# Kernel tuning notes

Hardware: AMD Instinct MI355X
Metric: run time of the kernel (lower is better)

The kernel has to match this reference:

```python
import jax, jax.numpy as jnp
import numpy as np
import math

B, S, D, H = 4, 2048, 1024, 16
DK = D // H

def setup_inputs() -> dict:
    key = jax.random.key(0)
    ks = jax.random.split(key, 8)
    scale = 1.0 / math.sqrt(D)
    q = jax.random.normal(ks[0], (B, S, D), dtype=jnp.float32)
    k = jax.random.normal(ks[1], (B, S, D), dtype=jnp.float32)
    v = jax.random.normal(ks[2], (B, S, D), dtype=jnp.float32)
    Wq = jax.random.normal(ks[3], (D, D), dtype=jnp.float32) * scale
    Wk = jax.random.normal(ks[4], (D, D), dtype=jnp.float32) * scale
    Wv = jax.random.normal(ks[5], (D, D), dtype=jnp.float32) * scale
    Wo = jax.random.normal(ks[6], (D, D), dtype=jnp.float32) * scale
    # causal mask, broadcast over batch and heads (masked_fill where mask == 0)
    mask = jnp.tril(jnp.ones((S, S), dtype=jnp.int32))[None, None, :, :]
    return {"q": q, "k": k, "v": v, "Wq": Wq, "Wk": Wk, "Wv": Wv, "Wo": Wo, "mask": mask}

def reference(q, k, v, Wq, Wk, Wv, Wo, mask):
    # Linear projections (nn.Linear: x @ W^T), split heads -> [B, H, S, DK]
    def split_heads(x, W):
        y = jnp.einsum('bsd,ed->bse', x, W)
        return y.reshape(x.shape[0], x.shape[1], H, DK).transpose(0, 2, 1, 3)
    qh = split_heads(q, Wq)
    kh = split_heads(k, Wk)
    vh = split_heads(v, Wv)
    scores = jnp.einsum('bhqd,bhkd->bhqk', qh, kh) / math.sqrt(DK)  # [B,H,S,S]
    scores = jnp.where(mask == 0, -jnp.inf, scores)
    p = jax.nn.softmax(scores, axis=-1)
    ctx = jnp.einsum('bhqk,bhkd->bhqd', p, vh)
    ctx = ctx.transpose(0, 2, 1, 3).reshape(q.shape[0], q.shape[1], H * DK)
    return jnp.einsum('bsd,ed->bse', ctx, Wo)
```

## Files before the change

### kernel.cpp

```cpp
#include <hip/hip_runtime.h>

#define BB 4
#define SS 2048
#define DD 1024
#define HH 16
#define DKK 64
#define MTOT (BB * SS)
#define QKV_N (MTOT * DD)
#define W_N (DD * DD)

typedef __attribute__((ext_vector_type(8))) short short8;
typedef __attribute__((ext_vector_type(4))) float f32x4;
typedef __attribute__((ext_vector_type(4))) unsigned short u16x4;
typedef unsigned short ushort_t;

#define GP(p) ((__attribute__((address_space(1))) void*)(p))
#define LP(p) ((__attribute__((address_space(3))) void*)(p))

#if __has_builtin(__builtin_amdgcn_exp2f)
#define EXP2(x) __builtin_amdgcn_exp2f(x)
#else
#define EXP2(x) __expf((x) * 0.6931471805599453f)
#endif
#define QSCALE 0.1803368801111204f

__device__ __forceinline__ ushort_t f2bf(float f) {
    union { float f; unsigned u; } c; c.f = f;
    unsigned r = c.u + 0x7fffu + ((c.u >> 16) & 1u);
    return (ushort_t)(r >> 16);
}

__global__ __launch_bounds__(256)
void cvt2(const float* __restrict__ s0, ushort_t* __restrict__ d0, int n0,
          const float* __restrict__ s1, ushort_t* __restrict__ d1, int n1)
{
    int i = (blockIdx.x * 256 + threadIdx.x) * 4;
    const float* s; ushort_t* d; int off;
    if (i < n0) { s = s0; d = d0; off = i; }
    else        { s = s1; d = d1; off = i - n0; if (off >= n1) return; }
    f32x4 x = *(const f32x4*)(s + off);
    u16x4 h;
    h[0] = f2bf(x[0]); h[1] = f2bf(x[1]); h[2] = f2bf(x[2]); h[3] = f2bf(x[3]);
    *(u16x4*)(d + off) = h;
}

template<int MODE>
__global__ __launch_bounds__(256, 3)
void gemm_db(const ushort_t* __restrict__ A, const ushort_t* __restrict__ W,
             void* __restrict__ out, float scale)
{
    __shared__ ushort_t As[2][128 * 32];
    __shared__ ushort_t Bs[2][128 * 32];

    const int tid  = threadIdx.x;
    const int lane = tid & 63;
    const int w    = tid >> 6;
    const int wm   = w >> 1, wn = w & 1;
    const int l15  = lane & 15, l4 = lane >> 4;
    const int m0   = blockIdx.x * 128;
    const int n0   = blockIdx.y * 128;

    f32x4 acc[4][4] = {};

    auto stage = [&](int kk, int buf) {
        #pragma unroll
        for (int i = 0; i < 2; ++i) {
            int c  = i * 256 + tid;
            int r  = c >> 2;
            int cb = (c & 3) ^ (r & 3);
            __builtin_amdgcn_global_load_lds(
                GP(A + (size_t)(m0 + r) * 1024 + kk + cb * 8), LP(&As[buf][c * 8]), 16, 0, 0);
            __builtin_amdgcn_global_load_lds(
                GP(W + (size_t)(n0 + r) * 1024 + kk + cb * 8), LP(&Bs[buf][c * 8]), 16, 0, 0);
        }
    };

    stage(0, 0);

    for (int it = 0; it < 32; ++it) {
        __syncthreads();
        const ushort_t* Ac = As[it & 1];
        const ushort_t* Bc = Bs[it & 1];
        if (it + 1 < 32) stage((it + 1) * 32, (it + 1) & 1);

        short8 bfr[4];
        #pragma unroll
        for (int ni = 0; ni < 4; ++ni) {
            int row = wn * 64 + ni * 16 + l15;
            bfr[ni] = *(const short8*)(Bc + (row * 4 + (l4 ^ (row & 3))) * 8);
        }
        #pragma unroll
        for (int mi = 0; mi < 4; ++mi) {
            int row = wm * 64 + mi * 16 + l15;
            short8 af = *(const short8*)(Ac + (row * 4 + (l4 ^ (row & 3))) * 8);
            #pragma unroll
            for (int ni = 0; ni < 4; ++ni)
                acc[mi][ni] = __builtin_amdgcn_mfma_f32_16x16x32_bf16(
                    af, bfr[ni], acc[mi][ni], 0, 0, 0);
        }
    }

    #pragma unroll
    for (int mi = 0; mi < 4; ++mi) {
        int rowb = m0 + wm * 64 + mi * 16 + l4 * 4;
        #pragma unroll
        for (int ni = 0; ni < 4; ++ni) {
            int n = n0 + wn * 64 + ni * 16 + l15;
            if constexpr (MODE == 0) {
                int h = n >> 6, dk = n & 63;
                #pragma unroll
                for (int r = 0; r < 4; ++r) {
                    int m = rowb + r, b = m >> 11, s = m & 2047;
                    ((ushort_t*)out)[(((size_t)(b * 16 + h) * 2048 + s) << 6) + dk] =
                        f2bf(acc[mi][ni][r] * scale);
                }
            } else if constexpr (MODE == 1) {
                int h = n >> 6, dk = n & 63;
                int b = rowb >> 11, s0v = rowb & 2047;
                u16x4 hh;
                #pragma unroll
                for (int r = 0; r < 4; ++r) hh[r] = f2bf(acc[mi][ni][r]);
                *(u16x4*)((ushort_t*)out + (((size_t)(b * 16 + h) << 6) + dk) * 2048 + s0v) = hh;
            } else {
                #pragma unroll
                for (int r = 0; r < 4; ++r)
                    ((float*)out)[(size_t)(rowb + r) * 1024 + n] = acc[mi][ni][r];
            }
        }
    }
}

__global__ __launch_bounds__(256, 2)
void attn_fwd5(const ushort_t* __restrict__ Qh, const ushort_t* __restrict__ Kh,
               const ushort_t* __restrict__ Vt, ushort_t* __restrict__ Ctx)
{
    __shared__ ushort_t Kl[2][64 * 64];
    __shared__ ushort_t Vl[2][64 * 64];
    __shared__ ushort_t Pl[4][32][72];

    const int tid  = threadIdx.x;
    const int lane = tid & 63;
    const int w    = tid >> 6;
    const int l15  = lane & 15, l4 = lane >> 4;
    const int idx  = blockIdx.x;
    const int qt   = 15 - (idx >> 6);
    const int bh   = idx & 63;
    const int b    = bh >> 4, h = bh & 15;
    const int q0   = qt * 128;
    const ushort_t* Qb = Qh + (size_t)bh * SS * DKK;
    const ushort_t* Kb = Kh + (size_t)bh * SS * DKK;
    const ushort_t* Vb = Vt + (size_t)bh * DKK * SS;

    short8 qf[2][2];
    #pragma unroll
    for (int qg = 0; qg < 2; ++qg)
        #pragma unroll
        for (int ks = 0; ks < 2; ++ks) {
            int row = q0 + w * 32 + qg * 16 + l15;
            qf[qg][ks] = *(const short8*)(Qb + (size_t)row * 64 + ks * 32 + l4 * 8);
        }

    f32x4 Ot[2][4] = {};
    float m_i[2], l_i[2];
    m_i[0] = m_i[1] = -__builtin_inff();
    l_i[0] = l_i[1] = 0.f;

    auto stage = [&](int k0, ushort_t* Kd, ushort_t* Vd) {
        #pragma unroll
        for (int i = 0; i < 2; ++i) {
            int c  = i * 256 + tid;
            int r  = c >> 3;
            int cb = (c & 7) ^ (r & 7);
            __builtin_amdgcn_global_load_lds(
                GP(Kb + (size_t)(k0 + r) * 64 + cb * 8), LP(Kd + c * 8), 16, 0, 0);
            __builtin_amdgcn_global_load_lds(
                GP(Vb + (size_t)r * 2048 + k0 + cb * 8), LP(Vd + c * 8), 16, 0, 0);
        }
    };

    const int nkt = 2 * qt + 2;
    const int wrow0 = q0 + w * 32;
    stage(0, Kl[0], Vl[0]);

    for (int kt = 0; kt < nkt; ++kt) {
        const int k0 = kt * 64;
        __syncthreads();
        const ushort_t* Kc = Kl[kt & 1];
        const ushort_t* Vc = Vl[kt & 1];
        if (kt + 1 < nkt)
            stage(k0 + 64, Kl[(kt + 1) & 1], Vl[(kt + 1) & 1]);

        f32x4 sc[2][4] = {};
        #pragma unroll
        for (int ni = 0; ni < 4; ++ni) {
            short8 kf0, kf1;
            {
                int r = ni * 16 + l15;
                kf0 = *(const short8*)(Kc + (r * 8 + ((0 + l4) ^ (r & 7))) * 8);
                kf1 = *(const short8*)(Kc + (r * 8 + ((4 + l4) ^ (r & 7))) * 8);
            }
            #pragma unroll
            for (int qg = 0; qg < 2; ++qg) {
                sc[qg][ni] = __builtin_amdgcn_mfma_f32_16x16x32_bf16(
                    kf0, qf[qg][0], sc[qg][ni], 0, 0, 0);
                sc[qg][ni] = __builtin_amdgcn_mfma_f32_16x16x32_bf16(
                    kf1, qf[qg][1], sc[qg][ni], 0, 0, 0);
            }
        }

        if (k0 + 63 > wrow0) {
            #pragma unroll
            for (int qg = 0; qg < 2; ++qg) {
                int qrow = wrow0 + qg * 16 + l15;
                #pragma unroll
                for (int ni = 0; ni < 4; ++ni)
                    #pragma unroll
                    for (int r = 0; r < 4; ++r) {
                        int kcol = k0 + ni * 16 + l4 * 4 + r;
                        if (kcol > qrow) sc[qg][ni][r] = -1.0e30f;
                    }
            }
        }

        #pragma unroll
        for (int qg = 0; qg < 2; ++qg) {
            float mx = sc[qg][0][0];
            #pragma unroll
            for (int ni = 0; ni < 4; ++ni)
                #pragma unroll
                for (int r = 0; r < 4; ++r) mx = fmaxf(mx, sc[qg][ni][r]);
            mx = fmaxf(mx, __shfl_xor(mx, 16, 64));
            mx = fmaxf(mx, __shfl_xor(mx, 32, 64));
            float mnew  = fmaxf(m_i[qg], mx);
            float alpha = EXP2(m_i[qg] - mnew);
            float rs = 0.f;
            #pragma unroll
            for (int ni = 0; ni < 4; ++ni)
                #pragma unroll
                for (int r = 0; r < 4; ++r) {
                    float p = EXP2(sc[qg][ni][r] - mnew);
                    sc[qg][ni][r] = p;
                    rs += p;
                }
            rs += __shfl_xor(rs, 16, 64);
            rs += __shfl_xor(rs, 32, 64);
            l_i[qg] = l_i[qg] * alpha + rs;
            m_i[qg] = mnew;
            #pragma unroll
            for (int nd = 0; nd < 4; ++nd)
                #pragma unroll
                for (int r = 0; r < 4; ++r) Ot[qg][nd][r] *= alpha;
        }

        #pragma unroll
        for (int qg = 0; qg < 2; ++qg) {
            int qr = qg * 16 + l15;
            #pragma unroll
            for (int ni = 0; ni < 4; ++ni) {
                u16x4 hh;
                #pragma unroll
                for (int r = 0; r < 4; ++r) hh[r] = f2bf(sc[qg][ni][r]);
                *(u16x4*)(&Pl[w][qr][ni * 16 + l4 * 4]) = hh;
            }
        }

        short8 pT[2][2];
        #pragma unroll
        for (int qg = 0; qg < 2; ++qg)
            #pragma unroll
            for (int ks = 0; ks < 2; ++ks)
                pT[qg][ks] = *(const short8*)(&Pl[w][qg * 16 + l15][ks * 32 + l4 * 8]);

        #pragma unroll
        for (int nd = 0; nd < 4; ++nd) {
            short8 vf0, vf1;
            {
                int r = nd * 16 + l15;
                vf0 = *(const short8*)(Vc + (r * 8 + ((0 + l4) ^ (r & 7))) * 8);
                vf1 = *(const short8*)(Vc + (r * 8 + ((4 + l4) ^ (r & 7))) * 8);
            }
            #pragma unroll
            for (int qg = 0; qg < 2; ++qg) {
                Ot[qg][nd] = __builtin_amdgcn_mfma_f32_16x16x32_bf16(
                    vf0, pT[qg][0], Ot[qg][nd], 0, 0, 0);
                Ot[qg][nd] = __builtin_amdgcn_mfma_f32_16x16x32_bf16(
                    vf1, pT[qg][1], Ot[qg][nd], 0, 0, 0);
            }
        }
    }

    #pragma unroll
    for (int qg = 0; qg < 2; ++qg) {
        float inv = 1.0f / l_i[qg];
        int qrow = q0 + w * 32 + qg * 16 + l15;
        ushort_t* dst = Ctx + ((size_t)b * 2048 + qrow) * 1024 + h * 64;
        #pragma unroll
        for (int nd = 0; nd < 4; ++nd) {
            u16x4 hh;
            #pragma unroll
            for (int r = 0; r < 4; ++r) hh[r] = f2bf(Ot[qg][nd][r] * inv);
            *(u16x4*)(dst + nd * 16 + l4 * 4) = hh;
        }
    }
}

extern "C" void kernel_launch(void* const* d_in, const int* in_sizes, int n_in,
                              void* d_out, int out_size, void* d_ws, size_t ws_size,
                              hipStream_t stream)
{
    const float* q  = (const float*)d_in[0];
    const float* k  = (const float*)d_in[1];
    const float* v  = (const float*)d_in[2];
    const float* Wq = (const float*)d_in[3];
    const float* Wk = (const float*)d_in[4];
    const float* Wv = (const float*)d_in[5];
    const float* Wo = (const float*)d_in[6];
    float* out = (float*)d_out;

    ushort_t* B0 = (ushort_t*)d_ws;
    ushort_t* B1 = B0 + (size_t)QKV_N;
    ushort_t* B2 = B1 + (size_t)QKV_N;
    ushort_t* B3 = B2 + (size_t)QKV_N;
    ushort_t* wbE = (ushort_t*)d_out;
    dim3 gg(MTOT / 128, DD / 128);
    const int cvtg = (QKV_N + W_N) / 1024;

    cvt2<<<cvtg, 256, 0, stream>>>(q, B0, QKV_N, Wq, wbE, W_N);
    gemm_db<0><<<gg, 256, 0, stream>>>(B0, wbE, B1, QSCALE);

    cvt2<<<cvtg, 256, 0, stream>>>(k, B0, QKV_N, Wk, wbE, W_N);
    gemm_db<0><<<gg, 256, 0, stream>>>(B0, wbE, B2, 1.0f);

    cvt2<<<cvtg, 256, 0, stream>>>(v, B0, QKV_N, Wv, wbE, W_N);
    gemm_db<1><<<gg, 256, 0, stream>>>(B0, wbE, B3, 1.0f);

    attn_fwd5<<<1024, 256, 0, stream>>>(B1, B2, B3, B0);

    cvt2<<<W_N / 1024, 256, 0, stream>>>(Wo, B1, W_N, Wo, B1, 0);
    gemm_db<2><<<gg, 256, 0, stream>>>(B0, B1, out, 1.0f);
}
```

Measured before the change: 340.4 us.

## Batch QKV projections into one GEMM launch and convert fp32 weights inside the GEMM

The three activation fp32->bf16 conversions are merged into one kernel, and the Q/K/V projections into one GEMM launch over a 192x8 grid that picks its input, weight and output layout per segment. The separate weight-conversion kernels are removed: each GEMM now stages fp32 weight tiles into LDS with a new swizzle and packs them to bf16 in registers before the MFMA. This cuts kernel launches and the serial cvt/GEMM dependencies, and gives the projection GEMM a larger grid. In exchange the B-side tile doubles its LDS footprint and global traffic, and every block repeats the weight conversion. Q and K now live in the output buffer as scratch space until the final GEMM overwrites it.

```diff
diff --git a/kernel.cpp b/kernel.cpp
--- a/kernel.cpp
+++ b/kernel.cpp
@@ -30,102 +30,176 @@
     return (ushort_t)(r >> 16);
 }
 
+__device__ __forceinline__ short8 pack8(f32x4 lo, f32x4 hi) {
+    short8 r;
+    r[0] = (short)f2bf(lo[0]); r[1] = (short)f2bf(lo[1]);
+    r[2] = (short)f2bf(lo[2]); r[3] = (short)f2bf(lo[3]);
+    r[4] = (short)f2bf(hi[0]); r[5] = (short)f2bf(hi[1]);
+    r[6] = (short)f2bf(hi[2]); r[7] = (short)f2bf(hi[3]);
+    return r;
+}
+
 __global__ __launch_bounds__(256)
-void cvt2(const float* __restrict__ s0, ushort_t* __restrict__ d0, int n0,
-          const float* __restrict__ s1, ushort_t* __restrict__ d1, int n1)
+void cvt3(const float* __restrict__ q, const float* __restrict__ k,
+          const float* __restrict__ v, ushort_t* __restrict__ qb,
+          ushort_t* __restrict__ kb, ushort_t* __restrict__ vb)
 {
-    int i = (blockIdx.x * 256 + threadIdx.x) * 4;
-    const float* s; ushort_t* d; int off;
-    if (i < n0) { s = s0; d = d0; off = i; }
-    else        { s = s1; d = d1; off = i - n0; if (off >= n1) return; }
+    size_t i = ((size_t)blockIdx.x * 256 + threadIdx.x) * 4;
+    int seg = (int)(i >> 23);
+    size_t off = i & (size_t)(QKV_N - 1);
+    const float* s = (seg == 0) ? q : (seg == 1) ? k : v;
+    ushort_t*    d = (seg == 0) ? qb : (seg == 1) ? kb : vb;
     f32x4 x = *(const f32x4*)(s + off);
     u16x4 h;
     h[0] = f2bf(x[0]); h[1] = f2bf(x[1]); h[2] = f2bf(x[2]); h[3] = f2bf(x[3]);
     *(u16x4*)(d + off) = h;
 }
 
-template<int MODE>
-__global__ __launch_bounds__(256, 3)
-void gemm_db(const ushort_t* __restrict__ A, const ushort_t* __restrict__ W,
-             void* __restrict__ out, float scale)
-{
-    __shared__ ushort_t As[2][128 * 32];
-    __shared__ ushort_t Bs[2][128 * 32];
-
-    const int tid  = threadIdx.x;
-    const int lane = tid & 63;
-    const int w    = tid >> 6;
-    const int wm   = w >> 1, wn = w & 1;
-    const int l15  = lane & 15, l4 = lane >> 4;
-    const int m0   = blockIdx.x * 128;
-    const int n0   = blockIdx.y * 128;
-
-    f32x4 acc[4][4] = {};
-
-    auto stage = [&](int kk, int buf) {
+struct GemmCore {
+    const ushort_t* A; const float* W;
+    int m0, n0, tid, lane, w, wm, wn, l15, l4;
+    ushort_t (*As)[128 * 32];
+    float    (*Bsf)[128 * 32];
+
+    __device__ __forceinline__ void stage(int kk, int buf) {
         #pragma unroll
         for (int i = 0; i < 2; ++i) {
             int c  = i * 256 + tid;
             int r  = c >> 2;
             int cb = (c & 3) ^ (r & 3);
             __builtin_amdgcn_global_load_lds(
-                GP(A + (size_t)(m0 + r) * 1024 + kk + cb * 8), LP(&As[buf][c * 8]), 16, 0, 0);
+                GP(A + (size_t)(m0 + r) * 1024 + kk + cb * 8),
+                LP(&As[buf][c * 8]), 16, 0, 0);
+        }
+        #pragma unroll
+        for (int i = 0; i < 4; ++i) {
+            int c  = i * 256 + tid;
+            int r  = c >> 3;
+            int cb = (c & 7) ^ (r & 7);
             __builtin_amdgcn_global_load_lds(
-                GP(W + (size_t)(n0 + r) * 1024 + kk + cb * 8), LP(&Bs[buf][c * 8]), 16, 0, 0);
-        }
-    };
-
-    stage(0, 0);
-
-    for (int it = 0; it < 32; ++it) {
-        __syncthreads();
-        const ushort_t* Ac = As[it & 1];
-        const ushort_t* Bc = Bs[it & 1];
-        if (it + 1 < 32) stage((it + 1) * 32, (it + 1) & 1);
-
-        short8 bfr[4];
-        #pragma unroll
-        for (int ni = 0; ni < 4; ++ni) {
-            int row = wn * 64 + ni * 16 + l15;
-            bfr[ni] = *(const short8*)(Bc + (row * 4 + (l4 ^ (row & 3))) * 8);
-        }
-        #pragma unroll
-        for (int mi = 0; mi < 4; ++mi) {
-            int row = wm * 64 + mi * 16 + l15;
-            short8 af = *(const short8*)(Ac + (row * 4 + (l4 ^ (row & 3))) * 8);
-            #pragma unroll
-            for (int ni = 0; ni < 4; ++ni)
-                acc[mi][ni] = __builtin_amdgcn_mfma_f32_16x16x32_bf16(
-                    af, bfr[ni], acc[mi][ni], 0, 0, 0);
-        }
-    }
+                GP(W + (size_t)(n0 + r) * 1024 + kk + cb * 4),
+                LP(&Bsf[buf][c * 4]), 16, 0, 0);
+        }
+    }
+
+    __device__ __forceinline__ void run(f32x4 (&acc)[4][4]) {
+        stage(0, 0);
+        for (int it = 0; it < 32; ++it) {
+            __syncthreads();
+            const ushort_t* Ac = As[it & 1];
+            const float*    Bc = Bsf[it & 1];
+            if (it + 1 < 32) stage((it + 1) * 32, (it + 1) & 1);
+
+            short8 bfr[4];
+            #pragma unroll
+            for (int ni = 0; ni < 4; ++ni) {
+                int row = wn * 64 + ni * 16 + l15;
+                f32x4 lo = *(const f32x4*)(&Bc[(row * 8 + ((l4 * 2)     ^ (row & 7))) * 4]);
+                f32x4 hi = *(const f32x4*)(&Bc[(row * 8 + ((l4 * 2 + 1) ^ (row & 7))) * 4]);
+                bfr[ni] = pack8(lo, hi);
+            }
+            #pragma unroll
+            for (int mi = 0; mi < 4; ++mi) {
+                int row = wm * 64 + mi * 16 + l15;
+                short8 af = *(const short8*)(Ac + (row * 4 + (l4 ^ (row & 3))) * 8);
+                #pragma unroll
+                for (int ni = 0; ni < 4; ++ni)
+                    acc[mi][ni] = __builtin_amdgcn_mfma_f32_16x16x32_bf16(
+                        af, bfr[ni], acc[mi][ni], 0, 0, 0);
+            }
+        }
+    }
+};
+
+__global__ __launch_bounds__(256, 3)
+void gemm_qkv(const ushort_t* __restrict__ qb, const ushort_t* __restrict__ kb,
+              const ushort_t* __restrict__ vb, const float* __restrict__ Wq,
+              const float* __restrict__ Wk, const float* __restrict__ Wv,
+              ushort_t* __restrict__ Qh, ushort_t* __restrict__ Kh,
+              ushort_t* __restrict__ Vt)
+{
+    __shared__ ushort_t As[2][128 * 32];
+    __shared__ float    Bsf[2][128 * 32];
+
+    const int tid  = threadIdx.x;
+    const int lane = tid & 63;
+    const int w    = tid >> 6;
+    const int seg  = blockIdx.x >> 6;
+    const int mb   = blockIdx.x & 63;
+
+    GemmCore core;
+    core.A   = (seg == 0) ? qb : (seg == 1) ? kb : vb;
+    core.W   = (seg == 0) ? Wq : (seg == 1) ? Wk : Wv;
+    core.m0  = mb * 128;
+    core.n0  = blockIdx.y * 128;
+    core.tid = tid; core.lane = lane; core.w = w;
+    core.wm  = w >> 1; core.wn = w & 1;
+    core.l15 = lane & 15; core.l4 = lane >> 4;
+    core.As  = As; core.Bsf = Bsf;
+
+    f32x4 acc[4][4] = {};
+    core.run(acc);
+
+    const float scale = (seg == 0) ? QSCALE : 1.0f;
+    ushort_t* outHM = (seg == 0) ? Qh : Kh;
 
     #pragma unroll
     for (int mi = 0; mi < 4; ++mi) {
-        int rowb = m0 + wm * 64 + mi * 16 + l4 * 4;
+        int rowb = core.m0 + core.wm * 64 + mi * 16 + core.l4 * 4;
         #pragma unroll
         for (int ni = 0; ni < 4; ++ni) {
-            int n = n0 + wn * 64 + ni * 16 + l15;
-            if constexpr (MODE == 0) {
-                int h = n >> 6, dk = n & 63;
+            int n = core.n0 + core.wn * 64 + ni * 16 + core.l15;
+            int h = n >> 6, dk = n & 63;
+            if (seg < 2) {
                 #pragma unroll
                 for (int r = 0; r < 4; ++r) {
                     int m = rowb + r, b = m >> 11, s = m & 2047;
-                    ((ushort_t*)out)[(((size_t)(b * 16 + h) * 2048 + s) << 6) + dk] =
+                    outHM[(((size_t)(b * 16 + h) * 2048 + s) << 6) + dk] =
                         f2bf(acc[mi][ni][r] * scale);
                 }
-            } else if constexpr (MODE == 1) {
-                int h = n >> 6, dk = n & 63;
+            } else {
                 int b = rowb >> 11, s0v = rowb & 2047;
                 u16x4 hh;
                 #pragma unroll
                 for (int r = 0; r < 4; ++r) hh[r] = f2bf(acc[mi][ni][r]);
-                *(u16x4*)((ushort_t*)out + (((size_t)(b * 16 + h) << 6) + dk) * 2048 + s0v) = hh;
-            } else {
-                #pragma unroll
-                for (int r = 0; r < 4; ++r)
-                    ((float*)out)[(size_t)(rowb + r) * 1024 + n] = acc[mi][ni][r];
-            }
+                *(u16x4*)(Vt + (((size_t)(b * 16 + h) << 6) + dk) * 2048 + s0v) = hh;
+            }
+        }
+    }
+}
+
+__global__ __launch_bounds__(256, 3)
+void gemm_out(const ushort_t* __restrict__ Ctx, const float* __restrict__ Wo,
+              float* __restrict__ out)
+{
+    __shared__ ushort_t As[2][128 * 32];
+    __shared__ float    Bsf[2][128 * 32];
+
+    const int tid  = threadIdx.x;
+    const int lane = tid & 63;
+    const int w    = tid >> 6;
+
+    GemmCore core;
+    core.A   = Ctx;  core.W = Wo;
+    core.m0  = blockIdx.x * 128;
+    core.n0  = blockIdx.y * 128;
+    core.tid = tid; core.lane = lane; core.w = w;
+    core.wm  = w >> 1; core.wn = w & 1;
+    core.l15 = lane & 15; core.l4 = lane >> 4;
+    core.As  = As; core.Bsf = Bsf;
+
+    f32x4 acc[4][4] = {};
+    core.run(acc);
+
+    #pragma unroll
+    for (int mi = 0; mi < 4; ++mi) {
+        int rowb = core.m0 + core.wm * 64 + mi * 16 + core.l4 * 4;
+        #pragma unroll
+        for (int ni = 0; ni < 4; ++ni) {
+            int n = core.n0 + core.wn * 64 + ni * 16 + core.l15;
+            #pragma unroll
+            for (int r = 0; r < 4; ++r)
+                out[(size_t)(rowb + r) * 1024 + n] = acc[mi][ni][r];
         }
     }
 }
@@ -317,25 +391,16 @@
     const float* Wo = (const float*)d_in[6];
     float* out = (float*)d_out;
 
-    ushort_t* B0 = (ushort_t*)d_ws;
-    ushort_t* B1 = B0 + (size_t)QKV_N;
-    ushort_t* B2 = B1 + (size_t)QKV_N;
-    ushort_t* B3 = B2 + (size_t)QKV_N;
-    ushort_t* wbE = (ushort_t*)d_out;
-    dim3 gg(MTOT / 128, DD / 128);
-    const int cvtg = (QKV_N + W_N) / 1024;
-
-    cvt2<<<cvtg, 256, 0, stream>>>(q, B0, QKV_N, Wq, wbE, W_N);
-    gemm_db<0><<<gg, 256, 0, stream>>>(B0, wbE, B1, QSCALE);
-
-    cvt2<<<cvtg, 256, 0, stream>>>(k, B0, QKV_N, Wk, wbE, W_N);
-    gemm_db<0><<<gg, 256, 0, stream>>>(B0, wbE, B2, 1.0f);
-
-    cvt2<<<cvtg, 256, 0, stream>>>(v, B0, QKV_N, Wv, wbE, W_N);
-    gemm_db<1><<<gg, 256, 0, stream>>>(B0, wbE, B3, 1.0f);
-
-    attn_fwd5<<<1024, 256, 0, stream>>>(B1, B2, B3, B0);
-
-    cvt2<<<W_N / 1024, 256, 0, stream>>>(Wo, B1, W_N, Wo, B1, 0);
-    gemm_db<2><<<gg, 256, 0, stream>>>(B0, B1, out, 1.0f);
-}
+    ushort_t* qb  = (ushort_t*)d_ws;
+    ushort_t* kb  = qb + (size_t)QKV_N;
+    ushort_t* vb  = kb + (size_t)QKV_N;
+    ushort_t* Vt  = vb + (size_t)QKV_N;
+    ushort_t* Ctx = qb;
+    ushort_t* Qh  = (ushort_t*)d_out;
+    ushort_t* Kh  = Qh + (size_t)QKV_N;
+
+    cvt3<<<3 * QKV_N / 1024, 256, 0, stream>>>(q, k, v, qb, kb, vb);
+    gemm_qkv<<<dim3(192, 8), 256, 0, stream>>>(qb, kb, vb, Wq, Wk, Wv, Qh, Kh, Vt);
+    attn_fwd5<<<1024, 256, 0, stream>>>(Qh, Kh, Vt, Ctx);
+    gemm_out<<<dim3(64, 8), 256, 0, stream>>>(Ctx, Wo, out);
+}
```

New measurement: 373.1 us. 1.1x slower.

## Fuse activation bf16 conversion into a single batched QKV GEMM launch

Applied to the files above, without the earlier changes.

Removes the three separate fp32->bf16 conversion passes over q/k/v. The new QKV GEMM loads fp32 activations straight into LDS and packs them to bf16 in registers. The three projections now run as one launch with a 192x8 grid, and all four weight conversions happen in one kernel. The output projection uses 128x64 tiles at higher occupancy, and the attention launch bounds go up to 3 blocks per SM. This saves a lot of global traffic and launch overhead, at the cost of twice the LDS for the A tile and extra conversion ALU work in the GEMM inner loop. Q and K scratch buffers now live in the output buffer.

```diff
diff --git a/kernel.cpp b/kernel.cpp
--- a/kernel.cpp
+++ b/kernel.cpp
@@ -30,27 +30,129 @@
     return (ushort_t)(r >> 16);
 }
 
+__device__ __forceinline__ short8 pack8(f32x4 lo, f32x4 hi) {
+    short8 r;
+    r[0] = (short)f2bf(lo[0]); r[1] = (short)f2bf(lo[1]);
+    r[2] = (short)f2bf(lo[2]); r[3] = (short)f2bf(lo[3]);
+    r[4] = (short)f2bf(hi[0]); r[5] = (short)f2bf(hi[1]);
+    r[6] = (short)f2bf(hi[2]); r[7] = (short)f2bf(hi[3]);
+    return r;
+}
+
 __global__ __launch_bounds__(256)
-void cvt2(const float* __restrict__ s0, ushort_t* __restrict__ d0, int n0,
-          const float* __restrict__ s1, ushort_t* __restrict__ d1, int n1)
+void cvtW(const float* __restrict__ Wq, const float* __restrict__ Wk,
+          const float* __restrict__ Wv, const float* __restrict__ Wo,
+          ushort_t* __restrict__ dst)
 {
     int i = (blockIdx.x * 256 + threadIdx.x) * 4;
-    const float* s; ushort_t* d; int off;
-    if (i < n0) { s = s0; d = d0; off = i; }
-    else        { s = s1; d = d1; off = i - n0; if (off >= n1) return; }
+    int seg = i >> 20;
+    int off = i & (W_N - 1);
+    const float* s = (seg == 0) ? Wq : (seg == 1) ? Wk : (seg == 2) ? Wv : Wo;
     f32x4 x = *(const f32x4*)(s + off);
     u16x4 h;
     h[0] = f2bf(x[0]); h[1] = f2bf(x[1]); h[2] = f2bf(x[2]); h[3] = f2bf(x[3]);
-    *(u16x4*)(d + off) = h;
-}
-
-template<int MODE>
+    *(u16x4*)(dst + i) = h;
+}
+
 __global__ __launch_bounds__(256, 3)
-void gemm_db(const ushort_t* __restrict__ A, const ushort_t* __restrict__ W,
-             void* __restrict__ out, float scale)
+void gemm_qkv(const float* __restrict__ q, const float* __restrict__ k,
+              const float* __restrict__ v, const ushort_t* __restrict__ wb,
+              ushort_t* __restrict__ Qh, ushort_t* __restrict__ Kh,
+              ushort_t* __restrict__ Vt)
+{
+    __shared__ float    Asf[2][128 * 32];
+    __shared__ ushort_t Bs [2][128 * 32];
+
+    const int tid  = threadIdx.x;
+    const int lane = tid & 63;
+    const int w    = tid >> 6;
+    const int wm   = w >> 1, wn = w & 1;
+    const int l15  = lane & 15, l4 = lane >> 4;
+    const int seg  = blockIdx.x >> 6;
+    const int m0   = (blockIdx.x & 63) * 128;
+    const int n0   = blockIdx.y * 128;
+    const float* A = (seg == 0) ? q : (seg == 1) ? k : v;
+    const ushort_t* W = wb + (size_t)seg * W_N;
+
+    auto stage = [&](int kk, int buf) {
+        #pragma unroll
+        for (int i = 0; i < 4; ++i) {
+            int c = i * 256 + tid, r = c >> 3, cb = (c & 7) ^ (r & 7);
+            __builtin_amdgcn_global_load_lds(
+                GP(A + (size_t)(m0 + r) * 1024 + kk + cb * 4),
+                LP(&Asf[buf][c * 4]), 16, 0, 0);
+        }
+        #pragma unroll
+        for (int i = 0; i < 2; ++i) {
+            int c = i * 256 + tid, r = c >> 2, cb = (c & 3) ^ ((r >> 1) & 3);
+            __builtin_amdgcn_global_load_lds(
+                GP(W + (size_t)(n0 + r) * 1024 + kk + cb * 8),
+                LP(&Bs[buf][c * 8]), 16, 0, 0);
+        }
+    };
+
+    f32x4 acc[4][4] = {};
+    stage(0, 0);
+
+    for (int it = 0; it < 32; ++it) {
+        __syncthreads();
+        const float*    Ac = Asf[it & 1];
+        const ushort_t* Bc = Bs[it & 1];
+        if (it + 1 < 32) stage((it + 1) * 32, (it + 1) & 1);
+
+        short8 bfr[4];
+        #pragma unroll
+        for (int ni = 0; ni < 4; ++ni) {
+            int row = wn * 64 + ni * 16 + l15;
+            bfr[ni] = *(const short8*)(Bc + (row * 4 + (l4 ^ ((row >> 1) & 3))) * 8);
+        }
+        #pragma unroll
+        for (int mi = 0; mi < 4; ++mi) {
+            int row = wm * 64 + mi * 16 + l15;
+            f32x4 lo = *(const f32x4*)(&Ac[(row * 8 + ((l4 * 2)     ^ (row & 7))) * 4]);
+            f32x4 hi = *(const f32x4*)(&Ac[(row * 8 + ((l4 * 2 + 1) ^ (row & 7))) * 4]);
+            short8 af = pack8(lo, hi);
+            #pragma unroll
+            for (int ni = 0; ni < 4; ++ni)
+                acc[mi][ni] = __builtin_amdgcn_mfma_f32_16x16x32_bf16(
+                    af, bfr[ni], acc[mi][ni], 0, 0, 0);
+        }
+    }
+
+    const float scale = (seg == 0) ? QSCALE : 1.0f;
+    ushort_t* outHM = (seg == 0) ? Qh : Kh;
+
+    #pragma unroll
+    for (int mi = 0; mi < 4; ++mi) {
+        int rowb = m0 + wm * 64 + mi * 16 + l4 * 4;
+        #pragma unroll
+        for (int ni = 0; ni < 4; ++ni) {
+            int n = n0 + wn * 64 + ni * 16 + l15;
+            int h = n >> 6, dk = n & 63;
+            if (seg < 2) {
+                #pragma unroll
+                for (int r = 0; r < 4; ++r) {
+                    int m = rowb + r, b = m >> 11, s = m & 2047;
+                    outHM[(((size_t)(b * 16 + h) * 2048 + s) << 6) + dk] =
+                        f2bf(acc[mi][ni][r] * scale);
+                }
+            } else {
+                int b = rowb >> 11, s0v = rowb & 2047;
+                u16x4 hh;
+                #pragma unroll
+                for (int r = 0; r < 4; ++r) hh[r] = f2bf(acc[mi][ni][r]);
+                *(u16x4*)(Vt + (((size_t)(b * 16 + h) << 6) + dk) * 2048 + s0v) = hh;
+            }
+        }
+    }
+}
+
+__global__ __launch_bounds__(256, 4)
+void gemm_out(const ushort_t* __restrict__ Ctx, const ushort_t* __restrict__ wo,
+              float* __restrict__ out)
 {
     __shared__ ushort_t As[2][128 * 32];
-    __shared__ ushort_t Bs[2][128 * 32];
+    __shared__ ushort_t Bs[2][64 * 32];
 
     const int tid  = threadIdx.x;
     const int lane = tid & 63;
@@ -58,23 +160,25 @@
     const int wm   = w >> 1, wn = w & 1;
     const int l15  = lane & 15, l4 = lane >> 4;
     const int m0   = blockIdx.x * 128;
-    const int n0   = blockIdx.y * 128;
-
-    f32x4 acc[4][4] = {};
+    const int n0   = blockIdx.y * 64;
 
     auto stage = [&](int kk, int buf) {
         #pragma unroll
         for (int i = 0; i < 2; ++i) {
-            int c  = i * 256 + tid;
-            int r  = c >> 2;
-            int cb = (c & 3) ^ (r & 3);
-            __builtin_amdgcn_global_load_lds(
-                GP(A + (size_t)(m0 + r) * 1024 + kk + cb * 8), LP(&As[buf][c * 8]), 16, 0, 0);
-            __builtin_amdgcn_global_load_lds(
-                GP(W + (size_t)(n0 + r) * 1024 + kk + cb * 8), LP(&Bs[buf][c * 8]), 16, 0, 0);
+            int c = i * 256 + tid, r = c >> 2, cb = (c & 3) ^ ((r >> 1) & 3);
+            __builtin_amdgcn_global_load_lds(
+                GP(Ctx + (size_t)(m0 + r) * 1024 + kk + cb * 8),
+                LP(&As[buf][c * 8]), 16, 0, 0);
+        }
+        {
+            int c = tid, r = c >> 2, cb = (c & 3) ^ ((r >> 1) & 3);
+            __builtin_amdgcn_global_load_lds(
+                GP(wo + (size_t)(n0 + r) * 1024 + kk + cb * 8),
+                LP(&Bs[buf][c * 8]), 16, 0, 0);
         }
     };
 
+    f32x4 acc[4][2] = {};
     stage(0, 0);
 
     for (int it = 0; it < 32; ++it) {
@@ -83,18 +187,18 @@
         const ushort_t* Bc = Bs[it & 1];
         if (it + 1 < 32) stage((it + 1) * 32, (it + 1) & 1);
 
-        short8 bfr[4];
-        #pragma unroll
-        for (int ni = 0; ni < 4; ++ni) {
-            int row = wn * 64 + ni * 16 + l15;
-            bfr[ni] = *(const short8*)(Bc + (row * 4 + (l4 ^ (row & 3))) * 8);
+        short8 bfr[2];
+        #pragma unroll
+        for (int ni = 0; ni < 2; ++ni) {
+            int row = wn * 32 + ni * 16 + l15;
+            bfr[ni] = *(const short8*)(Bc + (row * 4 + (l4 ^ ((row >> 1) & 3))) * 8);
         }
         #pragma unroll
         for (int mi = 0; mi < 4; ++mi) {
             int row = wm * 64 + mi * 16 + l15;
-            short8 af = *(const short8*)(Ac + (row * 4 + (l4 ^ (row & 3))) * 8);
-            #pragma unroll
-            for (int ni = 0; ni < 4; ++ni)
+            short8 af = *(const short8*)(Ac + (row * 4 + (l4 ^ ((row >> 1) & 3))) * 8);
+            #pragma unroll
+            for (int ni = 0; ni < 2; ++ni)
                 acc[mi][ni] = __builtin_amdgcn_mfma_f32_16x16x32_bf16(
                     af, bfr[ni], acc[mi][ni], 0, 0, 0);
         }
@@ -104,33 +208,16 @@
     for (int mi = 0; mi < 4; ++mi) {
         int rowb = m0 + wm * 64 + mi * 16 + l4 * 4;
         #pragma unroll
-        for (int ni = 0; ni < 4; ++ni) {
-            int n = n0 + wn * 64 + ni * 16 + l15;
-            if constexpr (MODE == 0) {
-                int h = n >> 6, dk = n & 63;
-                #pragma unroll
-                for (int r = 0; r < 4; ++r) {
-                    int m = rowb + r, b = m >> 11, s = m & 2047;
-                    ((ushort_t*)out)[(((size_t)(b * 16 + h) * 2048 + s) << 6) + dk] =
-                        f2bf(acc[mi][ni][r] * scale);
-                }
-            } else if constexpr (MODE == 1) {
-                int h = n >> 6, dk = n & 63;
-                int b = rowb >> 11, s0v = rowb & 2047;
-                u16x4 hh;
-                #pragma unroll
-                for (int r = 0; r < 4; ++r) hh[r] = f2bf(acc[mi][ni][r]);
-                *(u16x4*)((ushort_t*)out + (((size_t)(b * 16 + h) << 6) + dk) * 2048 + s0v) = hh;
-            } else {
-                #pragma unroll
-                for (int r = 0; r < 4; ++r)
-                    ((float*)out)[(size_t)(rowb + r) * 1024 + n] = acc[mi][ni][r];
-            }
-        }
-    }
-}
-
-__global__ __launch_bounds__(256, 2)
+        for (int ni = 0; ni < 2; ++ni) {
+            int n = n0 + wn * 32 + ni * 16 + l15;
+            #pragma unroll
+            for (int r = 0; r < 4; ++r)
+                out[(size_t)(rowb + r) * 1024 + n] = acc[mi][ni][r];
+        }
+    }
+}
+
+__global__ __launch_bounds__(256, 3)
 void attn_fwd5(const ushort_t* __restrict__ Qh, const ushort_t* __restrict__ Kh,
                const ushort_t* __restrict__ Vt, ushort_t* __restrict__ Ctx)
 {
@@ -317,25 +404,14 @@
     const float* Wo = (const float*)d_in[6];
     float* out = (float*)d_out;
 
-    ushort_t* B0 = (ushort_t*)d_ws;
-    ushort_t* B1 = B0 + (size_t)QKV_N;
-    ushort_t* B2 = B1 + (size_t)QKV_N;
-    ushort_t* B3 = B2 + (size_t)QKV_N;
-    ushort_t* wbE = (ushort_t*)d_out;
-    dim3 gg(MTOT / 128, DD / 128);
-    const int cvtg = (QKV_N + W_N) / 1024;
-
-    cvt2<<<cvtg, 256, 0, stream>>>(q, B0, QKV_N, Wq, wbE, W_N);
-    gemm_db<0><<<gg, 256, 0, stream>>>(B0, wbE, B1, QSCALE);
-
-    cvt2<<<cvtg, 256, 0, stream>>>(k, B0, QKV_N, Wk, wbE, W_N);
-    gemm_db<0><<<gg, 256, 0, stream>>>(B0, wbE, B2, 1.0f);
-
-    cvt2<<<cvtg, 256, 0, stream>>>(v, B0, QKV_N, Wv, wbE, W_N);
-    gemm_db<1><<<gg, 256, 0, stream>>>(B0, wbE, B3, 1.0f);
-
-    attn_fwd5<<<1024, 256, 0, stream>>>(B1, B2, B3, B0);
-
-    cvt2<<<W_N / 1024, 256, 0, stream>>>(Wo, B1, W_N, Wo, B1, 0);
-    gemm_db<2><<<gg, 256, 0, stream>>>(B0, B1, out, 1.0f);
-}
+    ushort_t* wb  = (ushort_t*)d_ws;
+    ushort_t* Vt  = wb + (size_t)4 * W_N;
+    ushort_t* Ctx = Vt + (size_t)QKV_N;
+    ushort_t* Qh  = (ushort_t*)d_out;
+    ushort_t* Kh  = Qh + (size_t)QKV_N;
+
+    cvtW<<<4 * W_N / 1024, 256, 0, stream>>>(Wq, Wk, Wv, Wo, wb);
+    gemm_qkv<<<dim3(192, 8), 256, 0, stream>>>(q, k, v, wb, Qh, Kh, Vt);
+    attn_fwd5<<<1024, 256, 0, stream>>>(Qh, Kh, Vt, Ctx);
+    gemm_out<<<dim3(64, 16), 256, 0, stream>>>(Ctx, wb + (size_t)3 * W_N, out);
+}
```

New measurement: 327.8 us. -3.7%, faster.
